# Kernel tuning notes

Hardware: AMD Instinct MI355X
Metric: run time of the kernel (lower is better)

The kernel has to match this reference:

```python
import jax, jax.numpy as jnp
import numpy as np

B, N, D, K = 64, 512, 256, 1024
LIMIT = float(np.sqrt(K))   # default initialize_limit = num_embeddings ** 0.5
BN_EPS = 1e-5               # torch BatchNorm1d default eps


def setup_inputs() -> dict:
    key = jax.random.key(0)
    k1, k2, k3 = jax.random.split(key, 3)
    x = jax.random.normal(k1, (B, N, D), jnp.float32)
    atom_mask = jax.random.randint(k2, (B, N), 0, 2, jnp.int32)
    e_i_ts = jax.random.uniform(k3, (D, K), jnp.float32, -LIMIT, LIMIT)
    return {
        "x": x,
        "atom_mask": atom_mask,
        "e_i_ts": e_i_ts,
        "bn_gamma": jnp.ones((D,), jnp.float32),
        "bn_beta": jnp.zeros((D,), jnp.float32),
    }


def reference(x, atom_mask, e_i_ts, bn_gamma, bn_beta):
    flat = x.reshape(-1, D)                          # [BN, D]
    m = atom_mask.reshape(-1).astype(flat.dtype)     # [BN], 1 = valid atom
    n_valid = jnp.maximum(m.sum(), 1.0)

    # BatchNorm1d (training mode) over valid atoms only (torch applies BN to
    # the gathered rows). Biased variance, as in torch's normalization.
    mu = (m[:, None] * flat).sum(0) / n_valid
    var = (m[:, None] * (flat - mu) ** 2).sum(0) / n_valid
    xb = (flat - mu) * jax.lax.rsqrt(var + BN_EPS) * bn_gamma + bn_beta

    # squared-distance to codebook + argmin + gather
    d = (xb ** 2).sum(1, keepdims=True) - 2.0 * (xb @ e_i_ts) + (e_i_ts ** 2).sum(0, keepdims=True)  # [BN, K]
    idx = jnp.argmin(d, axis=1)                      # [BN]
    q = e_i_ts.T[idx]                                # [BN, D] quantized (valid-row semantics)

    # scatter back into padded tensor (padded rows -> 0), straight-through
    q_pad = (m[:, None] * q).reshape(x.shape)
    quantized_x = x + jax.lax.stop_gradient(q_pad - x)

    sg = jax.lax.stop_gradient
    dictionary_loss = (m[:, None] * (sg(xb) - q) ** 2).sum() / (n_valid * D)
    commitment_loss = (m[:, None] * (xb - sg(q)) ** 2).sum() / (n_valid * D)

    # perplexity over valid atoms
    counts = jnp.zeros((K,), flat.dtype).at[idx].add(m)
    avg_probs = counts / n_valid
    perplexity = jnp.exp(-jnp.sum(avg_probs * jnp.log(avg_probs + 1e-10)))

    idx_out = jnp.where(m > 0, idx, -1)[:, None]     # [BN, 1]; -1 marks padded rows
    return quantized_x, dictionary_loss, commitment_loss, idx_out, perplexity
```

## Files before the change

### kernel.cpp

```cpp
#include <hip/hip_runtime.h>
#include <math.h>

#define BN   32768
#define DIM  256
#define KC   1024
#define BN_EPS 1e-5f

#define QX_SIZE   (BN * DIM)
#define LOSS0_OFF (QX_SIZE)
#define LOSS1_OFF (QX_SIZE + 1)
#define IDX_OFF   (QX_SIZE + 2)
#define PERP_OFF  (QX_SIZE + 2 + BN)

#define WS_SUM    0
#define WS_SUMSQ  256
#define WS_COUNT  512
#define WS_LOSS   513
#define WS_COUNTS 1024
#define WS_CNORM  3072
#define WS_EBH    8192
#define WS_EBL    (8192 + 131072)
#define WS_ETP    (8192 + 262144)
#define WS_ET_LEG 8192

typedef short bf16x8  __attribute__((ext_vector_type(8)));
typedef short short4v __attribute__((ext_vector_type(4)));
typedef float f32x4   __attribute__((ext_vector_type(4)));
typedef float fvec4   __attribute__((ext_vector_type(4)));
typedef int   int4v   __attribute__((ext_vector_type(4)));

static __device__ inline unsigned short f2bf(float f) {
    unsigned int u = __float_as_uint(f);
    return (unsigned short)((u + 0x7FFFu + ((u >> 16) & 1u)) >> 16);
}
static __device__ inline float bf2f(short s) {
    return __uint_as_float(((unsigned int)(unsigned short)s) << 16);
}
static __device__ inline fvec4 nt_ld4(const void* p) {
    return __builtin_nontemporal_load((const fvec4*)p);
}
static __device__ inline void nt_st(float* p, float v) {
    __builtin_nontemporal_store(v, p);
}

__global__ __launch_bounds__(256) void k_pre(const float* __restrict__ x,
                                             const int* __restrict__ mask,
                                             const float* __restrict__ e,
                                             float* __restrict__ ws,
                                             int use_et, int use_pk, int et_off) {
    int t = threadIdx.x;
    int b = blockIdx.x;
    if (b >= 260) {
        if (!use_et) return;
        int b2 = b - 260;
        int d0 = (b2 >> 4) * 64;
        int k0 = (b2 & 15) * 64;
        __shared__ float tile[64][65];
        int c = t & 63;
        int rq = t >> 6;
        #pragma unroll
        for (int p = 0; p < 16; ++p) {
            int dd = p * 4 + rq;
            tile[dd][c] = e[(size_t)(d0 + dd) * KC + k0 + c];
        }
        __syncthreads();
        #pragma unroll
        for (int p = 0; p < 16; ++p) {
            int kk = p * 4 + rq;
            nt_st(&ws[et_off + (size_t)(k0 + kk) * DIM + d0 + c], tile[c][kk]);
        }
        if (use_pk) {
            short* pbh = (short*)(ws + WS_EBH);
            short* pbl = (short*)(ws + WS_EBL);
            int lane2 = t & 63;
            int g = t >> 6;
            int quad2 = lane2 >> 4, col2 = lane2 & 15;
            #pragma unroll
            for (int f = 0; f < 2; ++f) {
                int fi = g * 2 + f;
                int ctl = fi >> 1, kcl = fi & 1;
                int ct = (b2 & 15) * 4 + ctl;
                int kc = (b2 >> 4) * 2 + kcl;
                bf16x8 hv, lv;
                #pragma unroll
                for (int j = 0; j < 8; ++j) {
                    float v = tile[kcl * 32 + quad2 * 8 + j][ctl * 16 + col2];
                    unsigned u = __float_as_uint(v);
                    hv[j] = (short)(u >> 16);
                    float lf = v - __uint_as_float(u & 0xffff0000u);
                    lv[j] = (short)(__float_as_uint(lf) >> 16);
                }
                size_t fb = ((size_t)(ct * 8 + kc) * 64 + lane2) * 8;
                *(bf16x8*)(pbh + fb) = hv;
                *(bf16x8*)(pbl + fb) = lv;
            }
        }
        return;
    }
    if (b >= 256) {
        int k = (b - 256) * 256 + t;
        float acc = 0.f;
        #pragma unroll 8
        for (int d = 0; d < DIM; ++d) {
            float v = e[(size_t)d * KC + k];
            acc = fmaf(v, v, acc);
        }
        ws[WS_CNORM + k] = acc;
        return;
    }
    __shared__ float s4[4 * 256];
    __shared__ float q4[4 * 256];
    __shared__ float cntS[4];
    int c4 = t & 63;
    int rsub = t >> 6;
    float s0=0.f,s1=0.f,s2=0.f,s3=0.f, q0=0.f,q1=0.f,q2=0.f,q3=0.f, cnt=0.f;
    int rbase = b * 4 + rsub;
    for (int i = 0; i < 32; ++i) {
        int r = rbase + i * 1024;
        float m = (float)mask[r];
        fvec4 v = nt_ld4(&x[(size_t)r * DIM + c4 * 4]);
        cnt += m;
        float m0 = m*v.x, m1 = m*v.y, m2 = m*v.z, m3 = m*v.w;
        s0 += m0; s1 += m1; s2 += m2; s3 += m3;
        q0 = fmaf(m0, v.x, q0); q1 = fmaf(m1, v.y, q1);
        q2 = fmaf(m2, v.z, q2); q3 = fmaf(m3, v.w, q3);
    }
    int f = c4 * 4;
    s4[rsub * 256 + f + 0] = s0; s4[rsub * 256 + f + 1] = s1;
    s4[rsub * 256 + f + 2] = s2; s4[rsub * 256 + f + 3] = s3;
    q4[rsub * 256 + f + 0] = q0; q4[rsub * 256 + f + 1] = q1;
    q4[rsub * 256 + f + 2] = q2; q4[rsub * 256 + f + 3] = q3;
    if (c4 == 0) cntS[rsub] = cnt;
    __syncthreads();
    float stot = s4[t] + s4[256 + t] + s4[512 + t] + s4[768 + t];
    float qtot = q4[t] + q4[256 + t] + q4[512 + t] + q4[768 + t];
    atomicAdd(&ws[WS_SUM + t], stot);
    atomicAdd(&ws[WS_SUMSQ + t], qtot);
    if (t == 0)
        atomicAdd(&ws[WS_COUNT], cntS[0] + cntS[1] + cntS[2] + cntS[3]);
}

__global__ __launch_bounds__(512, 2) void k_main_mfma(
        const float* __restrict__ x, const int* __restrict__ mask,
        const float* __restrict__ e, const float* __restrict__ gamma,
        const float* __restrict__ beta,
        const float* __restrict__ ws, float* __restrict__ out,
        int use_et, int use_pk, int et_off) {
    __shared__ __align__(16) short afrag[8 * 4 * 2 * 64 * 8];
    __shared__ float muS[DIM], scS[DIM], btS[DIM];
    __shared__ float cnS[KC];
    __shared__ float redv[64 * 8];
    __shared__ int   redi[64 * 8];
    __shared__ int   idxS[64];
    __shared__ float mskS[64];
    __shared__ float wred[8];

    const int tid = threadIdx.x;
    const int row0 = blockIdx.x * 64;
    const int w = tid >> 6;
    const int lane = tid & 63;
    const int quad = lane >> 4;
    const int col0 = lane & 15;

    if (tid < 256) {
        float cnt = ws[WS_COUNT];
        float nv = fmaxf(cnt, 1.f);
        float mu = ws[WS_SUM + tid] / nv;
        float var = ws[WS_SUMSQ + tid] / nv - mu * mu;
        var = fmaxf(var, 0.f);
        muS[tid] = mu;
        scS[tid] = rsqrtf(var + BN_EPS) * gamma[tid];
        btS[tid] = beta[tid];
    }
    cnS[tid] = ws[WS_CNORM + tid];
    cnS[512 + tid] = ws[WS_CNORM + 512 + tid];
    __syncthreads();

    {
        const int mt = w >> 1;
        const float* xr = x + (size_t)(row0 + mt * 16 + col0) * DIM;
        const int kq = quad * 8;
        #pragma unroll
        for (int kk = 0; kk < 4; ++kk) {
            int kc = (w & 1) * 4 + kk;
            int k0 = kc * 32 + kq;
            fvec4 v0 = nt_ld4(xr + k0);
            fvec4 v1 = nt_ld4(xr + k0 + 4);
            float xv[8] = {v0.x, v0.y, v0.z, v0.w, v1.x, v1.y, v1.z, v1.w};
            bf16x8 hv, lv;
            #pragma unroll
            for (int j = 0; j < 8; ++j) {
                float xb = fmaf(xv[j] - muS[k0 + j], scS[k0 + j], btS[k0 + j]);
                unsigned short h = f2bf(xb);
                float hf = __uint_as_float((unsigned)h << 16);
                hv[j] = (short)h;
                lv[j] = (short)f2bf(xb - hf);
            }
            int base = (((kc * 4 + mt) * 2) * 64 + lane) * 8;
            *(bf16x8*)&afrag[base] = hv;
            *(bf16x8*)&afrag[base + 512] = lv;
        }
    }
    __syncthreads();

    f32x4 acc[4][4];
    #pragma unroll
    for (int mt = 0; mt < 4; ++mt)
        #pragma unroll
        for (int nt = 0; nt < 4; ++nt)
            acc[mt][nt] = (f32x4){0.f, 0.f, 0.f, 0.f};

    if (use_pk) {
        const short* __restrict__ pbh = (const short*)(ws + WS_EBH);
        const short* __restrict__ pbl = (const short*)(ws + WS_EBL);
        bf16x8 cbh[4], cbl[4], nbh[4], nbl[4];
        #pragma unroll
        for (int nt = 0; nt < 4; ++nt) {
            size_t fb = ((size_t)((w * 8 + nt) * 8) * 64 + lane) * 8;
            cbh[nt] = *(const bf16x8*)(pbh + fb);
            cbl[nt] = *(const bf16x8*)(pbl + fb);
        }
        #pragma unroll
        for (int ng2 = 0; ng2 < 2; ++ng2) {
            #pragma unroll
            for (int kc = 0; kc < 8; ++kc) {
                const int ci = ng2 * 8 + kc;
                if (ci < 15) {
                    const int nci = ci + 1;
                    const int nng = nci >> 3, nkc = nci & 7;
                    #pragma unroll
                    for (int nt = 0; nt < 4; ++nt) {
                        size_t fb = ((size_t)((w * 8 + nng * 4 + nt) * 8 + nkc)
                                     * 64 + lane) * 8;
                        nbh[nt] = *(const bf16x8*)(pbh + fb);
                        nbl[nt] = *(const bf16x8*)(pbl + fb);
                    }
                }
                __builtin_amdgcn_sched_barrier(0);
                bf16x8 ah[4], al[4];
                #pragma unroll
                for (int mt = 0; mt < 4; ++mt) {
                    int base = (((kc * 4 + mt) * 2) * 64 + lane) * 8;
                    ah[mt] = *(const bf16x8*)&afrag[base];
                    al[mt] = *(const bf16x8*)&afrag[base + 512];
                }
                __builtin_amdgcn_s_setprio(1);
                #pragma unroll
                for (int nt = 0; nt < 4; ++nt) {
                    #pragma unroll
                    for (int mt = 0; mt < 4; ++mt) {
                        acc[mt][nt] = __builtin_amdgcn_mfma_f32_16x16x32_bf16(
                            ah[mt], cbh[nt], acc[mt][nt], 0, 0, 0);
                        acc[mt][nt] = __builtin_amdgcn_mfma_f32_16x16x32_bf16(
                            ah[mt], cbl[nt], acc[mt][nt], 0, 0, 0);
                        acc[mt][nt] = __builtin_amdgcn_mfma_f32_16x16x32_bf16(
                            al[mt], cbh[nt], acc[mt][nt], 0, 0, 0);
                    }
                }
                __builtin_amdgcn_s_setprio(0);
                if (ci < 15) {
                    #pragma unroll
                    for (int nt = 0; nt < 4; ++nt) {
                        cbh[nt] = nbh[nt];
                        cbl[nt] = nbl[nt];
                    }
                }
            }
            #pragma unroll
            for (int mt = 0; mt < 4; ++mt) {
                #pragma unroll
                for (int r = 0; r < 4; ++r) {
                    float v = 3.4e38f; int ii = 0;
                    #pragma unroll
                    for (int nt = 0; nt < 4; ++nt) {
                        int kcode = w * 128 + ng2 * 64 + nt * 16 + col0;
                        float s = fmaf(-2.f, acc[mt][nt][r], cnS[kcode]);
                        if (s < v) { v = s; ii = kcode; }
                        acc[mt][nt][r] = 0.f;
                    }
                    #pragma unroll
                    for (int m2 = 1; m2 < 16; m2 <<= 1) {
                        float v2 = __shfl_xor(v, m2, 64);
                        int   i2 = __shfl_xor(ii, m2, 64);
                        if (v2 < v || (v2 == v && i2 < ii)) { v = v2; ii = i2; }
                    }
                    if (col0 == 0) {
                        int row = mt * 16 + quad * 4 + r;
                        if (ng2 == 0) {
                            redv[row * 8 + w] = v; redi[row * 8 + w] = ii;
                        } else {
                            float bvv = redv[row * 8 + w];
                            int   bii = redi[row * 8 + w];
                            if (v < bvv || (v == bvv && ii < bii)) {
                                redv[row * 8 + w] = v; redi[row * 8 + w] = ii;
                            }
                        }
                    }
                }
            }
        }
    } else {
        const float* ebase = e + quad * 8192 + w * 128 + col0;
        #pragma unroll
        for (int ng2 = 0; ng2 < 2; ++ng2) {
            #pragma unroll
            for (int kc = 0; kc < 8; ++kc) {
                bf16x8 ah[4], al[4];
                #pragma unroll
                for (int mt = 0; mt < 4; ++mt) {
                    int base = (((kc * 4 + mt) * 2) * 64 + lane) * 8;
                    ah[mt] = *(const bf16x8*)&afrag[base];
                    al[mt] = *(const bf16x8*)&afrag[base + 512];
                }
                const float* ep = ebase + kc * 32768 + ng2 * 64;
                #pragma unroll
                for (int nt = 0; nt < 4; ++nt) {
                    const float* epn = ep + nt * 16;
                    float bv[8];
                    #pragma unroll
                    for (int j = 0; j < 8; ++j)
                        bv[j] = epn[j * 1024];
                    int4v hw, lw;
                    #pragma unroll
                    for (int p = 0; p < 4; ++p) {
                        unsigned u0 = __float_as_uint(bv[2 * p]);
                        unsigned u1 = __float_as_uint(bv[2 * p + 1]);
                        hw[p] = (int)__builtin_amdgcn_perm(u1, u0, 0x07060302u);
                        float l0 = bv[2 * p]     - __uint_as_float(u0 & 0xffff0000u);
                        float l1 = bv[2 * p + 1] - __uint_as_float(u1 & 0xffff0000u);
                        lw[p] = (int)__builtin_amdgcn_perm(__float_as_uint(l1),
                                                           __float_as_uint(l0),
                                                           0x07060302u);
                    }
                    bf16x8 bh = __builtin_bit_cast(bf16x8, hw);
                    bf16x8 bl = __builtin_bit_cast(bf16x8, lw);
                    #pragma unroll
                    for (int mt = 0; mt < 4; ++mt) {
                        acc[mt][nt] = __builtin_amdgcn_mfma_f32_16x16x32_bf16(
                            ah[mt], bh, acc[mt][nt], 0, 0, 0);
                        acc[mt][nt] = __builtin_amdgcn_mfma_f32_16x16x32_bf16(
                            ah[mt], bl, acc[mt][nt], 0, 0, 0);
                        acc[mt][nt] = __builtin_amdgcn_mfma_f32_16x16x32_bf16(
                            al[mt], bh, acc[mt][nt], 0, 0, 0);
                    }
                }
            }
            #pragma unroll
            for (int mt = 0; mt < 4; ++mt) {
                #pragma unroll
                for (int r = 0; r < 4; ++r) {
                    float v = 3.4e38f; int ii = 0;
                    #pragma unroll
                    for (int nt = 0; nt < 4; ++nt) {
                        int kcode = w * 128 + ng2 * 64 + nt * 16 + col0;
                        float s = fmaf(-2.f, acc[mt][nt][r], cnS[kcode]);
                        if (s < v) { v = s; ii = kcode; }
                        acc[mt][nt][r] = 0.f;
                    }
                    #pragma unroll
                    for (int m2 = 1; m2 < 16; m2 <<= 1) {
                        float v2 = __shfl_xor(v, m2, 64);
                        int   i2 = __shfl_xor(ii, m2, 64);
                        if (v2 < v || (v2 == v && i2 < ii)) { v = v2; ii = i2; }
                    }
                    if (col0 == 0) {
                        int row = mt * 16 + quad * 4 + r;
                        if (ng2 == 0) {
                            redv[row * 8 + w] = v; redi[row * 8 + w] = ii;
                        } else {
                            float bvv = redv[row * 8 + w];
                            int   bii = redi[row * 8 + w];
                            if (v < bvv || (v == bvv && ii < bii)) {
                                redv[row * 8 + w] = v; redi[row * 8 + w] = ii;
                            }
                        }
                    }
                }
            }
        }
    }
    __syncthreads();
    if (tid < 64) {
        float bv = redv[tid * 8];
        int bi = redi[tid * 8];
        #pragma unroll
        for (int t2 = 1; t2 < 8; ++t2) {
            float v = redv[tid * 8 + t2];
            int ii = redi[tid * 8 + t2];
            if (v < bv || (v == bv && ii < bi)) { bv = v; bi = ii; }
        }
        int m = mask[row0 + tid];
        idxS[tid] = bi;
        mskS[tid] = (float)m;
        out[IDX_OFF + row0 + tid] = m ? (float)bi : -1.0f;
        if (m) atomicAdd((float*)&ws[WS_COUNTS + bi], 1.0f);
    }
    __syncthreads();

    if (use_et) {
        const float* et = ws + et_off;
        const int d0 = lane * 4;
        const int kc_e = lane >> 3;
        const int quad_e = (lane >> 1) & 3;
        const int joff = (lane & 1) * 4;
        float lacc = 0.f;
        #pragma unroll
        for (int rr = 0; rr < 8; ++rr) {
            const int r = w * 8 + rr;
            const float m = mskS[r];
            const int idx = idxS[r];
            fvec4 g = nt_ld4(&et[(size_t)idx * DIM + d0]);
            const int mt = r >> 4;
            const int lane_a = quad_e * 16 + (r & 15);
            const int base = (((kc_e * 4 + mt) * 2) * 64 + lane_a) * 8 + joff;
            short4v h4 = *(const short4v*)&afrag[base];
            short4v l4 = *(const short4v*)&afrag[base + 512];
            fvec4 q;
            float dsum = 0.f;
            #pragma unroll
            for (int i = 0; i < 4; ++i) {
                float xb = bf2f(h4[i]) + bf2f(l4[i]);
                float diff = xb - g[i];
                dsum = fmaf(diff, diff, dsum);
                q[i] = m * g[i];
            }
            lacc = fmaf(m, dsum, lacc);
            __builtin_nontemporal_store(q,
                (fvec4*)&out[(size_t)(row0 + r) * DIM + d0]);
        }
        #pragma unroll
        for (int off2 = 32; off2 > 0; off2 >>= 1)
            lacc += __shfl_down(lacc, off2, 64);
        if (lane == 0) wred[w] = lacc;
    } else {
        const int d = tid & 255;
        const int rbase2 = (tid >> 8) * 32;
        const int ekc = d >> 5;
        const int equad = (d >> 3) & 3;
        const int ej = d & 7;
        const float* erow = e + (size_t)d * KC;
        float lacc = 0.f;
        for (int rr = 0; rr < 32; ++rr) {
            int r = rbase2 + rr;
            float m = mskS[r];
            float q = (m != 0.f) ? erow[idxS[r]] : 0.f;
            int off = (((ekc * 4 + (r >> 4)) * 2) * 64 + equad * 16 + (r & 15)) * 8 + ej;
            float xb = bf2f(afrag[off]) + bf2f(afrag[off + 512]);
            float diff = xb - q;
            lacc = fmaf(m * diff, diff, lacc);
            nt_st(&out[(size_t)(row0 + r) * DIM + d], q);
        }
        #pragma unroll
        for (int off2 = 32; off2 > 0; off2 >>= 1)
            lacc += __shfl_down(lacc, off2, 64);
        if (lane == 0) wred[w] = lacc;
    }
    __syncthreads();
    if (tid == 0) {
        float s = 0.f;
        #pragma unroll
        for (int i = 0; i < 8; ++i) s += wred[i];
        atomicAdd((float*)&ws[WS_LOSS], s);
    }
}

__global__ __launch_bounds__(256) void k_final(const float* __restrict__ ws,
                                               float* __restrict__ out) {
    int t = threadIdx.x;
    __shared__ float wr[4];
    float nv = fmaxf(ws[WS_COUNT], 1.f);
    float acc = 0.f;
    for (int j = t; j < KC; j += 256) {
        float p = ws[WS_COUNTS + j] / nv;
        acc = fmaf(p, logf(p + 1e-10f), acc);
    }
    #pragma unroll
    for (int off = 32; off > 0; off >>= 1) acc += __shfl_down(acc, off, 64);
    if ((t & 63) == 0) wr[t >> 6] = acc;
    __syncthreads();
    if (t == 0) {
        float ent = wr[0] + wr[1] + wr[2] + wr[3];
        float loss = ws[WS_LOSS] / (nv * (float)DIM);
        out[LOSS0_OFF] = loss;
        out[LOSS1_OFF] = loss;
        out[PERP_OFF] = expf(-ent);
    }
}

extern "C" void kernel_launch(void* const* d_in, const int* in_sizes, int n_in,
                              void* d_out, int out_size, void* d_ws, size_t ws_size,
                              hipStream_t stream) {
    const float* x     = (const float*)d_in[0];
    const int*   amask = (const int*)d_in[1];
    const float* e     = (const float*)d_in[2];
    const float* gamma = (const float*)d_in[3];
    const float* beta  = (const float*)d_in[4];
    float* out = (float*)d_out;
    float* ws  = (float*)d_ws;

    size_t need_pk = (size_t)(WS_ETP + KC * DIM) * sizeof(float);
    size_t need_et = (size_t)(WS_ET_LEG + KC * DIM) * sizeof(float);
    int use_pk = ws_size >= need_pk;
    int use_et = use_pk ? 1 : (ws_size >= need_et ? 1 : 0);
    int et_off = use_pk ? WS_ETP : WS_ET_LEG;

    (void)hipMemsetAsync(d_ws, 0, 8192, stream);

    k_pre<<<324, 256, 0, stream>>>(x, amask, e, ws, use_et, use_pk, et_off);
    k_main_mfma<<<BN / 64, 512, 0, stream>>>(x, amask, e, gamma, beta, ws, out,
                                             use_et, use_pk, et_off);
    k_final<<<1, 256, 0, stream>>>(ws, out);
}
```

Baseline: 261.2 us.

## Split gather/loss epilogue into separate kernel and halve main-kernel row tile

The main MFMA kernel now handles 32 rows per block with 256 threads (4 waves, each covering 256 codes) instead of 64 rows with 512 threads. Its launch bound targets 3 blocks per CU, shrinking LDS and accumulators. The quantized-row gather, output store and loss accumulation move into a new k_epi kernel. That kernel re-reads x and recomputes the batch-norm values rather than reusing the bf16 split fragments. This is meant to raise occupancy and shorten the argmin kernel's tail, at the cost of an extra launch, another full read of x, and each codebook fragment being reused across half as many rows.

Result: slower. 285.0 us (+9.1%).

```diff
diff --git a/kernel.cpp b/kernel.cpp
--- a/kernel.cpp
+++ b/kernel.cpp
@@ -24,7 +24,6 @@
 #define WS_ET_LEG 8192
 
 typedef short bf16x8  __attribute__((ext_vector_type(8)));
-typedef short short4v __attribute__((ext_vector_type(4)));
 typedef float f32x4   __attribute__((ext_vector_type(4)));
 typedef float fvec4   __attribute__((ext_vector_type(4)));
 typedef int   int4v   __attribute__((ext_vector_type(4)));
@@ -32,9 +31,6 @@
 static __device__ inline unsigned short f2bf(float f) {
     unsigned int u = __float_as_uint(f);
     return (unsigned short)((u + 0x7FFFu + ((u >> 16) & 1u)) >> 16);
-}
-static __device__ inline float bf2f(short s) {
-    return __uint_as_float(((unsigned int)(unsigned short)s) << 16);
 }
 static __device__ inline fvec4 nt_ld4(const void* p) {
     return __builtin_nontemporal_load((const fvec4*)p);
@@ -140,29 +136,25 @@
         atomicAdd(&ws[WS_COUNT], cntS[0] + cntS[1] + cntS[2] + cntS[3]);
 }
 
-__global__ __launch_bounds__(512, 2) void k_main_mfma(
+__global__ __launch_bounds__(256, 3) void k_main_mfma(
         const float* __restrict__ x, const int* __restrict__ mask,
         const float* __restrict__ e, const float* __restrict__ gamma,
         const float* __restrict__ beta,
-        const float* __restrict__ ws, float* __restrict__ out,
-        int use_et, int use_pk, int et_off) {
-    __shared__ __align__(16) short afrag[8 * 4 * 2 * 64 * 8];
+        const float* __restrict__ ws, float* __restrict__ out, int use_pk) {
+    __shared__ __align__(16) short afrag[8 * 2 * 2 * 64 * 8];
     __shared__ float muS[DIM], scS[DIM], btS[DIM];
     __shared__ float cnS[KC];
-    __shared__ float redv[64 * 8];
-    __shared__ int   redi[64 * 8];
-    __shared__ int   idxS[64];
-    __shared__ float mskS[64];
-    __shared__ float wred[8];
+    __shared__ float redv[32 * 4];
+    __shared__ int   redi[32 * 4];
 
     const int tid = threadIdx.x;
-    const int row0 = blockIdx.x * 64;
+    const int row0 = blockIdx.x * 32;
     const int w = tid >> 6;
     const int lane = tid & 63;
     const int quad = lane >> 4;
     const int col0 = lane & 15;
 
-    if (tid < 256) {
+    {
         float cnt = ws[WS_COUNT];
         float nv = fmaxf(cnt, 1.f);
         float mu = ws[WS_SUM + tid] / nv;
@@ -172,8 +164,9 @@
         scS[tid] = rsqrtf(var + BN_EPS) * gamma[tid];
         btS[tid] = beta[tid];
     }
-    cnS[tid] = ws[WS_CNORM + tid];
-    cnS[512 + tid] = ws[WS_CNORM + 512 + tid];
+    #pragma unroll
+    for (int p = 0; p < 4; ++p)
+        cnS[p * 256 + tid] = ws[WS_CNORM + p * 256 + tid];
     __syncthreads();
 
     {
@@ -196,16 +189,16 @@
                 hv[j] = (short)h;
                 lv[j] = (short)f2bf(xb - hf);
             }
-            int base = (((kc * 4 + mt) * 2) * 64 + lane) * 8;
+            int base = (((kc * 2 + mt) * 2) * 64 + lane) * 8;
             *(bf16x8*)&afrag[base] = hv;
             *(bf16x8*)&afrag[base + 512] = lv;
         }
     }
     __syncthreads();
 
-    f32x4 acc[4][4];
+    f32x4 acc[2][4];
     #pragma unroll
-    for (int mt = 0; mt < 4; ++mt)
+    for (int mt = 0; mt < 2; ++mt)
         #pragma unroll
         for (int nt = 0; nt < 4; ++nt)
             acc[mt][nt] = (f32x4){0.f, 0.f, 0.f, 0.f};
@@ -216,31 +209,31 @@
         bf16x8 cbh[4], cbl[4], nbh[4], nbl[4];
         #pragma unroll
         for (int nt = 0; nt < 4; ++nt) {
-            size_t fb = ((size_t)((w * 8 + nt) * 8) * 64 + lane) * 8;
+            size_t fb = ((size_t)((w * 16 + nt) * 8) * 64 + lane) * 8;
             cbh[nt] = *(const bf16x8*)(pbh + fb);
             cbl[nt] = *(const bf16x8*)(pbl + fb);
         }
         #pragma unroll
-        for (int ng2 = 0; ng2 < 2; ++ng2) {
+        for (int ng = 0; ng < 4; ++ng) {
             #pragma unroll
             for (int kc = 0; kc < 8; ++kc) {
-                const int ci = ng2 * 8 + kc;
-                if (ci < 15) {
+                const int ci = ng * 8 + kc;
+                if (ci < 31) {
                     const int nci = ci + 1;
                     const int nng = nci >> 3, nkc = nci & 7;
                     #pragma unroll
                     for (int nt = 0; nt < 4; ++nt) {
-                        size_t fb = ((size_t)((w * 8 + nng * 4 + nt) * 8 + nkc)
+                        size_t fb = ((size_t)((w * 16 + nng * 4 + nt) * 8 + nkc)
                                      * 64 + lane) * 8;
                         nbh[nt] = *(const bf16x8*)(pbh + fb);
                         nbl[nt] = *(const bf16x8*)(pbl + fb);
                     }
                 }
                 __builtin_amdgcn_sched_barrier(0);
-                bf16x8 ah[4], al[4];
-                #pragma unroll
-                for (int mt = 0; mt < 4; ++mt) {
-                    int base = (((kc * 4 + mt) * 2) * 64 + lane) * 8;
+                bf16x8 ah[2], al[2];
+                #pragma unroll
+                for (int mt = 0; mt < 2; ++mt) {
+                    int base = (((kc * 2 + mt) * 2) * 64 + lane) * 8;
                     ah[mt] = *(const bf16x8*)&afrag[base];
                     al[mt] = *(const bf16x8*)&afrag[base + 512];
                 }
@@ -248,7 +241,7 @@
                 #pragma unroll
                 for (int nt = 0; nt < 4; ++nt) {
                     #pragma unroll
-                    for (int mt = 0; mt < 4; ++mt) {
+                    for (int mt = 0; mt < 2; ++mt) {
                         acc[mt][nt] = __builtin_amdgcn_mfma_f32_16x16x32_bf16(
                             ah[mt], cbh[nt], acc[mt][nt], 0, 0, 0);
                         acc[mt][nt] = __builtin_amdgcn_mfma_f32_16x16x32_bf16(
@@ -258,7 +251,7 @@
                     }
                 }
                 __builtin_amdgcn_s_setprio(0);
-                if (ci < 15) {
+                if (ci < 31) {
                     #pragma unroll
                     for (int nt = 0; nt < 4; ++nt) {
                         cbh[nt] = nbh[nt];
@@ -267,13 +260,13 @@
                 }
             }
             #pragma unroll
-            for (int mt = 0; mt < 4; ++mt) {
+            for (int mt = 0; mt < 2; ++mt) {
                 #pragma unroll
                 for (int r = 0; r < 4; ++r) {
                     float v = 3.4e38f; int ii = 0;
                     #pragma unroll
                     for (int nt = 0; nt < 4; ++nt) {
-                        int kcode = w * 128 + ng2 * 64 + nt * 16 + col0;
+                        int kcode = w * 256 + ng * 64 + nt * 16 + col0;
                         float s = fmaf(-2.f, acc[mt][nt][r], cnS[kcode]);
                         if (s < v) { v = s; ii = kcode; }
                         acc[mt][nt][r] = 0.f;
@@ -286,13 +279,13 @@
                     }
                     if (col0 == 0) {
                         int row = mt * 16 + quad * 4 + r;
-                        if (ng2 == 0) {
-                            redv[row * 8 + w] = v; redi[row * 8 + w] = ii;
+                        if (ng == 0) {
+                            redv[row * 4 + w] = v; redi[row * 4 + w] = ii;
                         } else {
-                            float bvv = redv[row * 8 + w];
-                            int   bii = redi[row * 8 + w];
+                            float bvv = redv[row * 4 + w];
+                            int   bii = redi[row * 4 + w];
                             if (v < bvv || (v == bvv && ii < bii)) {
-                                redv[row * 8 + w] = v; redi[row * 8 + w] = ii;
+                                redv[row * 4 + w] = v; redi[row * 4 + w] = ii;
                             }
                         }
                     }
@@ -300,19 +293,19 @@
             }
         }
     } else {
-        const float* ebase = e + quad * 8192 + w * 128 + col0;
-        #pragma unroll
-        for (int ng2 = 0; ng2 < 2; ++ng2) {
+        const float* ebase = e + quad * 8192 + w * 256 + col0;
+        #pragma unroll
+        for (int ng = 0; ng < 4; ++ng) {
             #pragma unroll
             for (int kc = 0; kc < 8; ++kc) {
-                bf16x8 ah[4], al[4];
-                #pragma unroll
-                for (int mt = 0; mt < 4; ++mt) {
-                    int base = (((kc * 4 + mt) * 2) * 64 + lane) * 8;
+                bf16x8 ah[2], al[2];
+                #pragma unroll
+                for (int mt = 0; mt < 2; ++mt) {
+                    int base = (((kc * 2 + mt) * 2) * 64 + lane) * 8;
                     ah[mt] = *(const bf16x8*)&afrag[base];
                     al[mt] = *(const bf16x8*)&afrag[base + 512];
                 }
-                const float* ep = ebase + kc * 32768 + ng2 * 64;
+                const float* ep = ebase + kc * 32768 + ng * 64;
                 #pragma unroll
                 for (int nt = 0; nt < 4; ++nt) {
                     const float* epn = ep + nt * 16;
@@ -335,7 +328,7 @@
                     bf16x8 bh = __builtin_bit_cast(bf16x8, hw);
                     bf16x8 bl = __builtin_bit_cast(bf16x8, lw);
                     #pragma unroll
-                    for (int mt = 0; mt < 4; ++mt) {
+                    for (int mt = 0; mt < 2; ++mt) {
                         acc[mt][nt] = __builtin_amdgcn_mfma_f32_16x16x32_bf16(
                             ah[mt], bh, acc[mt][nt], 0, 0, 0);
                         acc[mt][nt] = __builtin_amdgcn_mfma_f32_16x16x32_bf16(
@@ -346,13 +339,13 @@
                 }
             }
             #pragma unroll
-            for (int mt = 0; mt < 4; ++mt) {
+            for (int mt = 0; mt < 2; ++mt) {
                 #pragma unroll
                 for (int r = 0; r < 4; ++r) {
                     float v = 3.4e38f; int ii = 0;
                     #pragma unroll
                     for (int nt = 0; nt < 4; ++nt) {
-                        int kcode = w * 128 + ng2 * 64 + nt * 16 + col0;
+                        int kcode = w * 256 + ng * 64 + nt * 16 + col0;
                         float s = fmaf(-2.f, acc[mt][nt][r], cnS[kcode]);
                         if (s < v) { v = s; ii = kcode; }
                         acc[mt][nt][r] = 0.f;
@@ -365,13 +358,13 @@
                     }
                     if (col0 == 0) {
                         int row = mt * 16 + quad * 4 + r;
-                        if (ng2 == 0) {
-                            redv[row * 8 + w] = v; redi[row * 8 + w] = ii;
+                        if (ng == 0) {
+                            redv[row * 4 + w] = v; redi[row * 4 + w] = ii;
                         } else {
-                            float bvv = redv[row * 8 + w];
-                            int   bii = redi[row * 8 + w];
+                            float bvv = redv[row * 4 + w];
+                            int   bii = redi[row * 4 + w];
                             if (v < bvv || (v == bvv && ii < bii)) {
-                                redv[row * 8 + w] = v; redi[row * 8 + w] = ii;
+                                redv[row * 4 + w] = v; redi[row * 4 + w] = ii;
                             }
                         }
                     }
@@ -380,88 +373,86 @@
         }
     }
     __syncthreads();
-    if (tid < 64) {
-        float bv = redv[tid * 8];
-        int bi = redi[tid * 8];
-        #pragma unroll
-        for (int t2 = 1; t2 < 8; ++t2) {
-            float v = redv[tid * 8 + t2];
-            int ii = redi[tid * 8 + t2];
+    if (tid < 32) {
+        float bv = redv[tid * 4];
+        int bi = redi[tid * 4];
+        #pragma unroll
+        for (int t2 = 1; t2 < 4; ++t2) {
+            float v = redv[tid * 4 + t2];
+            int ii = redi[tid * 4 + t2];
             if (v < bv || (v == bv && ii < bi)) { bv = v; bi = ii; }
         }
         int m = mask[row0 + tid];
-        idxS[tid] = bi;
-        mskS[tid] = (float)m;
         out[IDX_OFF + row0 + tid] = m ? (float)bi : -1.0f;
         if (m) atomicAdd((float*)&ws[WS_COUNTS + bi], 1.0f);
     }
-    __syncthreads();
-
-    if (use_et) {
-        const float* et = ws + et_off;
-        const int d0 = lane * 4;
-        const int kc_e = lane >> 3;
-        const int quad_e = (lane >> 1) & 3;
-        const int joff = (lane & 1) * 4;
-        float lacc = 0.f;
-        #pragma unroll
-        for (int rr = 0; rr < 8; ++rr) {
-            const int r = w * 8 + rr;
-            const float m = mskS[r];
-            const int idx = idxS[r];
-            fvec4 g = nt_ld4(&et[(size_t)idx * DIM + d0]);
-            const int mt = r >> 4;
-            const int lane_a = quad_e * 16 + (r & 15);
-            const int base = (((kc_e * 4 + mt) * 2) * 64 + lane_a) * 8 + joff;
-            short4v h4 = *(const short4v*)&afrag[base];
-            short4v l4 = *(const short4v*)&afrag[base + 512];
-            fvec4 q;
-            float dsum = 0.f;
-            #pragma unroll
-            for (int i = 0; i < 4; ++i) {
-                float xb = bf2f(h4[i]) + bf2f(l4[i]);
-                float diff = xb - g[i];
-                dsum = fmaf(diff, diff, dsum);
-                q[i] = m * g[i];
-            }
-            lacc = fmaf(m, dsum, lacc);
-            __builtin_nontemporal_store(q,
-                (fvec4*)&out[(size_t)(row0 + r) * DIM + d0]);
-        }
-        #pragma unroll
-        for (int off2 = 32; off2 > 0; off2 >>= 1)
-            lacc += __shfl_down(lacc, off2, 64);
-        if (lane == 0) wred[w] = lacc;
-    } else {
-        const int d = tid & 255;
-        const int rbase2 = (tid >> 8) * 32;
-        const int ekc = d >> 5;
-        const int equad = (d >> 3) & 3;
-        const int ej = d & 7;
-        const float* erow = e + (size_t)d * KC;
-        float lacc = 0.f;
-        for (int rr = 0; rr < 32; ++rr) {
-            int r = rbase2 + rr;
-            float m = mskS[r];
-            float q = (m != 0.f) ? erow[idxS[r]] : 0.f;
-            int off = (((ekc * 4 + (r >> 4)) * 2) * 64 + equad * 16 + (r & 15)) * 8 + ej;
-            float xb = bf2f(afrag[off]) + bf2f(afrag[off + 512]);
-            float diff = xb - q;
-            lacc = fmaf(m * diff, diff, lacc);
-            nt_st(&out[(size_t)(row0 + r) * DIM + d], q);
-        }
-        #pragma unroll
-        for (int off2 = 32; off2 > 0; off2 >>= 1)
-            lacc += __shfl_down(lacc, off2, 64);
-        if (lane == 0) wred[w] = lacc;
-    }
-    __syncthreads();
-    if (tid == 0) {
-        float s = 0.f;
-        #pragma unroll
-        for (int i = 0; i < 8; ++i) s += wred[i];
-        atomicAdd((float*)&ws[WS_LOSS], s);
-    }
+}
+
+__global__ __launch_bounds__(256) void k_epi(
+        const float* __restrict__ x, const int* __restrict__ mask,
+        const float* __restrict__ e, const float* __restrict__ gamma,
+        const float* __restrict__ beta,
+        const float* __restrict__ ws, float* __restrict__ out,
+        int use_et, int et_off) {
+    __shared__ __align__(16) float muS[DIM], scS[DIM], btS[DIM];
+    __shared__ float wred[4];
+    const int tid = threadIdx.x;
+    const int row0 = blockIdx.x * 32;
+    const int w = tid >> 6;
+    const int lane = tid & 63;
+    {
+        float cnt = ws[WS_COUNT];
+        float nv = fmaxf(cnt, 1.f);
+        float mu = ws[WS_SUM + tid] / nv;
+        float var = ws[WS_SUMSQ + tid] / nv - mu * mu;
+        var = fmaxf(var, 0.f);
+        muS[tid] = mu;
+        scS[tid] = rsqrtf(var + BN_EPS) * gamma[tid];
+        btS[tid] = beta[tid];
+    }
+    __syncthreads();
+
+    const int d0 = lane * 4;
+    fvec4 mu4 = *(const fvec4*)&muS[d0];
+    fvec4 sc4 = *(const fvec4*)&scS[d0];
+    fvec4 bt4 = *(const fvec4*)&btS[d0];
+    const float* et = ws + et_off;
+    float lacc = 0.f;
+    #pragma unroll
+    for (int rr = 0; rr < 8; ++rr) {
+        const int row = row0 + w * 8 + rr;
+        const int m = mask[row];
+        const float fm = (float)m;
+        const int idx = m ? (int)out[IDX_OFF + row] : 0;
+        fvec4 xv = nt_ld4(&x[(size_t)row * DIM + d0]);
+        fvec4 g;
+        if (use_et) {
+            g = nt_ld4(&et[(size_t)idx * DIM + d0]);
+        } else {
+            g.x = e[(size_t)(d0 + 0) * KC + idx];
+            g.y = e[(size_t)(d0 + 1) * KC + idx];
+            g.z = e[(size_t)(d0 + 2) * KC + idx];
+            g.w = e[(size_t)(d0 + 3) * KC + idx];
+        }
+        fvec4 q;
+        float dsum = 0.f;
+        #pragma unroll
+        for (int i = 0; i < 4; ++i) {
+            float xb = fmaf(xv[i] - mu4[i], sc4[i], bt4[i]);
+            float diff = xb - g[i];
+            dsum = fmaf(diff, diff, dsum);
+            q[i] = fm * g[i];
+        }
+        lacc = fmaf(fm, dsum, lacc);
+        __builtin_nontemporal_store(q, (fvec4*)&out[(size_t)row * DIM + d0]);
+    }
+    #pragma unroll
+    for (int off2 = 32; off2 > 0; off2 >>= 1)
+        lacc += __shfl_down(lacc, off2, 64);
+    if (lane == 0) wred[w] = lacc;
+    __syncthreads();
+    if (tid == 0)
+        atomicAdd((float*)&ws[WS_LOSS], wred[0] + wred[1] + wred[2] + wred[3]);
 }
 
 __global__ __launch_bounds__(256) void k_final(const float* __restrict__ ws,
@@ -507,7 +498,9 @@
     (void)hipMemsetAsync(d_ws, 0, 8192, stream);
 
     k_pre<<<324, 256, 0, stream>>>(x, amask, e, ws, use_et, use_pk, et_off);
-    k_main_mfma<<<BN / 64, 512, 0, stream>>>(x, amask, e, gamma, beta, ws, out,
-                                             use_et, use_pk, et_off);
+    k_main_mfma<<<BN / 32, 256, 0, stream>>>(x, amask, e, gamma, beta, ws, out,
+                                             use_pk);
+    k_epi<<<BN / 32, 256, 0, stream>>>(x, amask, e, gamma, beta, ws, out,
+                                       use_et, et_off);
     k_final<<<1, 256, 0, stream>>>(ws, out);
 }
```
